# Kernel optimization log

Hardware: AMD Instinct MI355X
Metric: run time of the kernel (lower is better)

Reference implementation:

```python
import jax, jax.numpy as jnp
import numpy as np

# ---- configuration matching init_kwargs ----
D_IN, D_HID, D_OUT = 4096, 4096, 4096
INTRINSIC = 1024            # size of trainable vector V
BATCH = 512
Q = float(min(np.log(60000.0) ** 2 / INTRINSIC, 1.0))  # fastJL_vars: q = min(ln(60000)^2/d, 1)

PARAM_SHAPES = {
    'W1': (D_HID, D_IN),   # nn.Linear weight is (out, in)
    'b1': (D_HID,),
    'W2': (D_OUT, D_HID),
    'b2': (D_OUT,),
}

def _next_pow2(n):
    return 1 << int(np.ceil(np.log2(n)))

def fwht(x):
    """Fast Walsh-Hadamard transform over a length-2^k vector.
    Mirrors fast_walsh_hadamard_torched: at step i, split axis i of the
    [2]*k view into halves a,b and concatenate (a+b, a-b)."""
    n = x.shape[0]
    steps = int(round(np.log2(n)))
    for i in range(steps):
        y = x.reshape(2 ** i, 2, -1)
        a, b = y[:, 0], y[:, 1]
        x = jnp.stack([a + b, a - b], axis=1).reshape(n)
    return x

def fastjl(V, D, PP, shape):
    """ret = (1/dd) * (PP * FWHT(D * pad(V, LL)))[:DD], reshaped to param shape."""
    LL = D.shape[0]
    dd = V.shape[0]
    DD = int(np.prod(shape))
    v_pad = jnp.zeros((LL,), V.dtype).at[:dd].set(V)
    h = fwht(D * v_pad)
    return ((PP * h)[:DD] / dd).reshape(shape)

def setup_inputs() -> dict:
    key = jax.random.key(0)
    ks = jax.random.split(key, 4 + 3 * len(PARAM_SHAPES) + len(PARAM_SHAPES))
    inp = {}
    inp['x'] = jax.random.normal(ks[0], (BATCH, D_IN), dtype=jnp.float32)
    inp['V'] = jax.random.normal(ks[1], (INTRINSIC,), dtype=jnp.float32) * 0.01
    i = 2
    for name, shape in PARAM_SHAPES.items():
        # initial (frozen) parameter values
        scale = 1.0 / np.sqrt(shape[-1]) if len(shape) > 1 else 0.0
        inp[name + '_init'] = jax.random.normal(ks[i], shape, dtype=jnp.float32) * scale
        LL = _next_pow2(int(np.prod(shape)))
        # D: Rademacher +-1
        rad = jax.random.bernoulli(ks[i + 1], 0.5, (LL,))
        inp['D_' + name] = jnp.where(rad, 1.0, -1.0).astype(jnp.float32)
        # PP = B * R, B ~ Bernoulli(1-q), R ~ N(0, (1/q)^2)
        B = jax.random.bernoulli(ks[i + 2], 1.0 - Q, (LL,)).astype(jnp.float32)
        R = jax.random.normal(ks[i + 3], (LL,), dtype=jnp.float32) * (1.0 / Q)
        inp['PP_' + name] = B * R
        i += 4
    return inp

def reference(x, V, W1_init, b1_init, W2_init, b2_init,
              D_W1, PP_W1, D_b1, PP_b1, D_W2, PP_W2, D_b2, PP_b2):
    # Reconstruct each wrapped-module parameter: init + FastJL(V)
    W1 = W1_init + fastjl(V, D_W1, PP_W1, PARAM_SHAPES['W1'])
    b1 = b1_init + fastjl(V, D_b1, PP_b1, PARAM_SHAPES['b1'])
    W2 = W2_init + fastjl(V, D_W2, PP_W2, PARAM_SHAPES['W2'])
    b2 = b2_init + fastjl(V, D_b2, PP_b2, PARAM_SHAPES['b2'])
    # wrapped module forward: Linear -> ReLU -> Linear
    h = jax.nn.relu(x @ W1.T + b1)
    return h @ W2.T + b2
```

## Files before the change

### kernel.cpp

```cpp
#include <hip/hip_runtime.h>
#include <hip/hip_bf16.h>
#include <stdint.h>

typedef unsigned short u16;
typedef __attribute__((ext_vector_type(8))) short short8;
typedef __attribute__((ext_vector_type(4))) float f32x4;

__device__ __forceinline__ uint32_t f2bf(float f) {
    union { float f; uint32_t u; } c; c.f = f;
    uint32_t u = c.u;
    u += 0x7fffu + ((u >> 16) & 1u);
    return u >> 16;
}

__device__ __forceinline__ void glds16(const void* g, void* l) {
    __builtin_amdgcn_global_load_lds(
        (const __attribute__((address_space(1))) uint32_t*)g,
        (__attribute__((address_space(3))) uint32_t*)l,
        16, 0, 0);
}

__device__ __forceinline__ uint2 wrow2(float4 wi, float4 pp, float4 gv) {
    uint32_t lo = f2bf(wi.x + pp.x * gv.x) | (f2bf(wi.y + pp.y * gv.y) << 16);
    uint32_t hi = f2bf(wi.z + pp.z * gv.z) | (f2bf(wi.w + pp.w * gv.w) << 16);
    return make_uint2(lo, hi);
}

__global__ void fwht_g_kernel(const float* __restrict__ V,
                              const float* __restrict__ D0, const float* __restrict__ D1,
                              const float* __restrict__ D2, const float* __restrict__ D3,
                              float* __restrict__ g) {
    __shared__ float s[1024];
    int t = threadIdx.x;
    const float* D = (blockIdx.x == 0) ? D0 : (blockIdx.x == 1) ? D1 :
                     (blockIdx.x == 2) ? D2 : D3;
    s[t] = D[t] * V[t];
    __syncthreads();
    #pragma unroll
    for (int st = 512; st >= 1; st >>= 1) {
        float a = s[t];
        float b = s[t ^ st];
        __syncthreads();
        s[t] = (t & st) ? (b - a) : (a + b);
        __syncthreads();
    }
    g[blockIdx.x * 1024 + t] = s[t] * (1.0f / 1024.0f);
}

__global__ void bias_kernel(const float* __restrict__ init, const float* __restrict__ PP,
                            const float* __restrict__ g, float* __restrict__ out, int n) {
    int i = blockIdx.x * blockDim.x + threadIdx.x;
    if (i < n) out[i] = init[i] + PP[i] * g[i & 1023];
}

__global__ void cast_kernel(const float* __restrict__ in, u16* __restrict__ out, int n4) {
    int i = blockIdx.x * blockDim.x + threadIdx.x;
    if (i >= n4) return;
    float4 v = ((const float4*)in)[i];
    uint32_t lo = f2bf(v.x) | (f2bf(v.y) << 16);
    uint32_t hi = f2bf(v.z) | (f2bf(v.w) << 16);
    ((uint2*)out)[i] = make_uint2(lo, hi);
}

__global__ __launch_bounds__(256, 2) void gemm_fused(const u16* __restrict__ A,
                                                     const float* __restrict__ Winit,
                                                     const float* __restrict__ PP,
                                                     const float* __restrict__ gvec,
                                                     float* __restrict__ P,
                                                     int M, int N, int K, int Kslice) {
    constexpr int BM = 256, BN = 64, BK = 64;
    __shared__ u16 As[2][BM * BK];
    __shared__ u16 Bs[2][BN * BK];

    const int t    = threadIdx.x;
    const int wid  = t >> 6;
    const int lane = t & 63;
    const int fr   = lane & 15;
    const int fq   = lane >> 4;
    const int rx   = (fr & 7) << 4;

    const int bn = blockIdx.x, bm = blockIdx.y, sk = blockIdx.z;
    const int k_beg = sk * Kslice;
    const int kmax  = k_beg + Kslice - BK;
    const int npair = (Kslice / BK) / 2;

    const u16* Abase = A + (size_t)(bm * BM) * K;

    const int rB  = t >> 4;
    const int cB  = (t & 15) * 4;
    const int cb8 = (t & 15) * 8;
    const int wxor = (rB & 7) << 4;
    const float* Wb = Winit + (size_t)(bn * BN + rB) * K;
    const float* Pb = PP    + (size_t)(bn * BN + rB) * K;
    const size_t rstride = (size_t)16 * K;

    float4 w00, w01, w02, w03, p00, p01, p02, p03;
    float4 w10, w11, w12, w13, p10, p11, p12, p13;

#define PF_W0(k0) do {                                        \
        const float* wp_ = Wb + (k0) + cB;                    \
        const float* qp_ = Pb + (k0) + cB;                    \
        w00 = *(const float4*)(wp_);                          \
        w01 = *(const float4*)(wp_ + rstride);                \
        w02 = *(const float4*)(wp_ + 2 * rstride);            \
        w03 = *(const float4*)(wp_ + 3 * rstride);            \
        p00 = *(const float4*)(qp_);                          \
        p01 = *(const float4*)(qp_ + rstride);                \
        p02 = *(const float4*)(qp_ + 2 * rstride);            \
        p03 = *(const float4*)(qp_ + 3 * rstride);            \
    } while (0)

#define PF_W1(k0) do {                                        \
        const float* wp_ = Wb + (k0) + cB;                    \
        const float* qp_ = Pb + (k0) + cB;                    \
        w10 = *(const float4*)(wp_);                          \
        w11 = *(const float4*)(wp_ + rstride);                \
        w12 = *(const float4*)(wp_ + 2 * rstride);            \
        w13 = *(const float4*)(wp_ + 3 * rstride);            \
        p10 = *(const float4*)(qp_);                          \
        p11 = *(const float4*)(qp_ + rstride);                \
        p12 = *(const float4*)(qp_ + 2 * rstride);            \
        p13 = *(const float4*)(qp_ + 3 * rstride);            \
    } while (0)

#define WRITE_B0(k0, buf) do {                                                    \
        float4 gv_ = *(const float4*)(gvec + (((k0) + cB) & 1023));               \
        char* Bp_ = (char*)Bs[buf];                                               \
        *(uint2*)(Bp_ + ((((rB +  0) * 128 + cb8)) ^ wxor)) = wrow2(w00, p00, gv_); \
        *(uint2*)(Bp_ + ((((rB + 16) * 128 + cb8)) ^ wxor)) = wrow2(w01, p01, gv_); \
        *(uint2*)(Bp_ + ((((rB + 32) * 128 + cb8)) ^ wxor)) = wrow2(w02, p02, gv_); \
        *(uint2*)(Bp_ + ((((rB + 48) * 128 + cb8)) ^ wxor)) = wrow2(w03, p03, gv_); \
    } while (0)

#define WRITE_B1(k0, buf) do {                                                    \
        float4 gv_ = *(const float4*)(gvec + (((k0) + cB) & 1023));               \
        char* Bp_ = (char*)Bs[buf];                                               \
        *(uint2*)(Bp_ + ((((rB +  0) * 128 + cb8)) ^ wxor)) = wrow2(w10, p10, gv_); \
        *(uint2*)(Bp_ + ((((rB + 16) * 128 + cb8)) ^ wxor)) = wrow2(w11, p11, gv_); \
        *(uint2*)(Bp_ + ((((rB + 32) * 128 + cb8)) ^ wxor)) = wrow2(w12, p12, gv_); \
        *(uint2*)(Bp_ + ((((rB + 48) * 128 + cb8)) ^ wxor)) = wrow2(w13, p13, gv_); \
    } while (0)

#define STAGE_A(k0, buf) do {                                                     \
        _Pragma("unroll")                                                         \
        for (int q_ = 0; q_ < 8; ++q_) {                                          \
            int L_ = q_ * 256 + t;                           \
            int row_ = L_ >> 3;                                                   \
            int cg_ = (L_ & 7) ^ (row_ & 7);              \
            glds16(Abase + (size_t)row_ * K + (k0) + cg_ * 8, As[buf] + L_ * 8);  \
        }                                                                         \
    } while (0)

#define MFMA_STEP(buf) do {                                                       \
        const char* Ap_ = (const char*)As[buf];                                   \
        const char* Bp_ = (const char*)Bs[buf];                                   \
        __builtin_amdgcn_s_setprio(1);                                            \
        _Pragma("unroll")                                                         \
        for (int ks_ = 0; ks_ < 2; ++ks_) {                                       \
            const int co_ = (ks_ * 64 + fq * 16) ^ rx;                            \
            short8 a_[4], b_[4];                                                  \
            _Pragma("unroll")                                                     \
            for (int m_ = 0; m_ < 4; ++m_)                                        \
                a_[m_] = *(const short8*)(Ap_ +                                   \
                          (wid * 64 + m_ * 16 + fr) * 128 + co_);                 \
            _Pragma("unroll")                                                     \
            for (int n_ = 0; n_ < 4; ++n_)                                        \
                b_[n_] = *(const short8*)(Bp_ + (n_ * 16 + fr) * 128 + co_);      \
            _Pragma("unroll")                                                     \
            for (int m_ = 0; m_ < 4; ++m_)                                        \
                _Pragma("unroll")                                                 \
                for (int n_ = 0; n_ < 4; ++n_)                                    \
                    acc[m_][n_] = __builtin_amdgcn_mfma_f32_16x16x32_bf16(        \
                        a_[m_], b_[n_], acc[m_][n_], 0, 0, 0);                    \
        }                                                                         \
        __builtin_amdgcn_s_setprio(0);                                            \
    } while (0)

#define WAIT_BAR() do {                                                           \
        asm volatile("s_waitcnt vmcnt(8) lgkmcnt(0)" ::: "memory");               \
        __builtin_amdgcn_s_barrier();                                             \
        __builtin_amdgcn_sched_barrier(0);                                        \
    } while (0)

    f32x4 acc[4][4];
    #pragma unroll
    for (int m = 0; m < 4; ++m)
        #pragma unroll
        for (int n = 0; n < 4; ++n)
            acc[m][n] = (f32x4){0.f, 0.f, 0.f, 0.f};

    PF_W0(k_beg);
    __builtin_amdgcn_sched_barrier(0);
    STAGE_A(k_beg, 0);
    __builtin_amdgcn_sched_barrier(0);
    PF_W1(k_beg + BK);
    __builtin_amdgcn_sched_barrier(0);
    WRITE_B0(k_beg, 0);
    WAIT_BAR();

    int kk = k_beg;
    #pragma unroll 1
    for (int p = 0; p < npair; ++p, kk += 2 * BK) {
        const int nk = kk + BK;
        int n2 = kk + 2 * BK; if (n2 > kmax) n2 = kmax;
        int n3 = kk + 3 * BK; if (n3 > kmax) n3 = kmax;

        STAGE_A(nk, 1);
        __builtin_amdgcn_sched_barrier(0);
        PF_W0(n2);
        __builtin_amdgcn_sched_barrier(0);
        MFMA_STEP(0);
        WRITE_B1(nk, 1);
        WAIT_BAR();

        STAGE_A(n2, 0);
        __builtin_amdgcn_sched_barrier(0);
        PF_W1(n3);
        __builtin_amdgcn_sched_barrier(0);
        MFMA_STEP(1);
        WRITE_B0(n2, 0);
        WAIT_BAR();
    }

#undef PF_W0
#undef PF_W1
#undef WRITE_B0
#undef WRITE_B1
#undef STAGE_A
#undef MFMA_STEP
#undef WAIT_BAR

    float* Pp = P + (size_t)sk * M * N;
    #pragma unroll
    for (int m = 0; m < 4; ++m) {
        int grow0 = bm * BM + wid * 64 + m * 16 + fq * 4;
        #pragma unroll
        for (int n = 0; n < 4; ++n) {
            int gcol = bn * BN + n * 16 + fr;
            #pragma unroll
            for (int j = 0; j < 4; ++j)
                Pp[(size_t)(grow0 + j) * N + gcol] = acc[m][n][j];
        }
    }
}

template <typename OutT, bool RELU, int S>
__global__ void reduce_kernel(const float* __restrict__ P, const float* __restrict__ bias,
                              OutT* __restrict__ out, int MN, int N) {
    int i = blockIdx.x * blockDim.x + threadIdx.x;
    if (i * 4 >= MN) return;
    int e = i * 4;
    int col = e & (N - 1);
    float4 acc = ((const float4*)(P + e))[0];
    #pragma unroll
    for (int s = 1; s < S; ++s) {
        float4 p = ((const float4*)(P + (size_t)s * MN + e))[0];
        acc.x += p.x; acc.y += p.y; acc.z += p.z; acc.w += p.w;
    }
    float4 bv = *((const float4*)(bias + col));
    acc.x += bv.x; acc.y += bv.y; acc.z += bv.z; acc.w += bv.w;
    if (RELU) {
        acc.x = fmaxf(acc.x, 0.f); acc.y = fmaxf(acc.y, 0.f);
        acc.z = fmaxf(acc.z, 0.f); acc.w = fmaxf(acc.w, 0.f);
    }
    if constexpr (sizeof(OutT) == 2) {
        uint32_t lo = f2bf(acc.x) | (f2bf(acc.y) << 16);
        uint32_t hi = f2bf(acc.z) | (f2bf(acc.w) << 16);
        ((uint2*)out)[i] = make_uint2(lo, hi);
    } else {
        ((float4*)out)[i] = acc;
    }
}

extern "C" void kernel_launch(void* const* d_in, const int* in_sizes, int n_in,
                              void* d_out, int out_size, void* d_ws, size_t ws_size,
                              hipStream_t stream) {
    (void)in_sizes; (void)n_in; (void)out_size; (void)ws_size;

    const float* x       = (const float*)d_in[0];
    const float* V       = (const float*)d_in[1];
    const float* W1_init = (const float*)d_in[2];
    const float* D_W1    = (const float*)d_in[3];
    const float* PP_W1   = (const float*)d_in[4];
    const float* b1_init = (const float*)d_in[5];
    const float* D_b1    = (const float*)d_in[6];
    const float* PP_b1   = (const float*)d_in[7];
    const float* W2_init = (const float*)d_in[8];
    const float* D_W2    = (const float*)d_in[9];
    const float* PP_W2   = (const float*)d_in[10];
    const float* b2_init = (const float*)d_in[11];
    const float* D_b2    = (const float*)d_in[12];
    const float* PP_b2   = (const float*)d_in[13];

    constexpr size_t MB = 1024 * 1024;
    char* ws = (char*)d_ws;
    float* g    = (float*)(ws);
    float* b1w  = (float*)(ws + 16384);
    float* b2w  = (float*)(ws + 32768);
    u16*   xb   = (u16*)(ws + 65536);
    u16*   hb   = (u16*)(ws + 65536 + 4 * MB);
    float* Pbuf = (float*)(ws + 65536 + 8 * MB);

    const int M = 512, N = 4096, K = 4096, S = 4, Kslice = K / S;

    fwht_g_kernel<<<4, 1024, 0, stream>>>(V, D_W1, D_b1, D_W2, D_b2, g);
    bias_kernel<<<4, 1024, 0, stream>>>(b1_init, PP_b1, g + 1024, b1w, 4096);
    bias_kernel<<<4, 1024, 0, stream>>>(b2_init, PP_b2, g + 3072, b2w, 4096);
    cast_kernel<<<2048, 256, 0, stream>>>(x, xb, M * K / 4);

    gemm_fused<<<dim3(N / 64, M / 256, S), 256, 0, stream>>>(xb, W1_init, PP_W1, g, Pbuf, M, N, K, Kslice);
    reduce_kernel<u16, true, S><<<M * N / 4 / 256, 256, 0, stream>>>(Pbuf, b1w, hb, M * N, N);

    gemm_fused<<<dim3(N / 64, M / 256, S), 256, 0, stream>>>(hb, W2_init, PP_W2, g + 2048, Pbuf, M, N, K, Kslice);
    reduce_kernel<float, false, S><<<M * N / 4 / 256, 256, 0, stream>>>(Pbuf, b2w, (float*)d_out, M * N, N);
}
```

Measured before the change: 130.1 us.

## Halve GEMM M-tile, single-buffer LDS, and raise occupancy to four blocks

Reduces the block tile from 256 to 128 rows, splits warps into a 2x2 layout over the 128x64 tile, and replaces the double-buffered LDS ping-pong with a single buffer guarded by two barriers per K step. Launch bounds are raised to four blocks per CU and the grid doubles in M. The intent is more resident blocks to hide latency, at the cost of each fp32 weight/PP tile being loaded and converted by twice as many blocks and losing the overlap of staging with MFMA.

```diff
diff --git a/kernel.cpp b/kernel.cpp
--- a/kernel.cpp
+++ b/kernel.cpp
@@ -62,27 +62,28 @@
     ((uint2*)out)[i] = make_uint2(lo, hi);
 }
 
-__global__ __launch_bounds__(256, 2) void gemm_fused(const u16* __restrict__ A,
+__global__ __launch_bounds__(256, 4) void gemm_fused(const u16* __restrict__ A,
                                                      const float* __restrict__ Winit,
                                                      const float* __restrict__ PP,
                                                      const float* __restrict__ gvec,
                                                      float* __restrict__ P,
                                                      int M, int N, int K, int Kslice) {
-    constexpr int BM = 256, BN = 64, BK = 64;
-    __shared__ u16 As[2][BM * BK];
-    __shared__ u16 Bs[2][BN * BK];
+    constexpr int BM = 128, BN = 64, BK = 64;
+    __shared__ u16 As[BM * BK];
+    __shared__ u16 Bs[BN * BK];
 
     const int t    = threadIdx.x;
     const int wid  = t >> 6;
     const int lane = t & 63;
+    const int wr   = wid >> 1;
+    const int wc   = wid & 1;
     const int fr   = lane & 15;
     const int fq   = lane >> 4;
     const int rx   = (fr & 7) << 4;
 
     const int bn = blockIdx.x, bm = blockIdx.y, sk = blockIdx.z;
     const int k_beg = sk * Kslice;
-    const int kmax  = k_beg + Kslice - BK;
-    const int npair = (Kslice / BK) / 2;
+    const int nstep = Kslice / BK;
 
     const u16* Abase = A + (size_t)(bm * BM) * K;
 
@@ -94,149 +95,108 @@
     const float* Pb = PP    + (size_t)(bn * BN + rB) * K;
     const size_t rstride = (size_t)16 * K;
 
-    float4 w00, w01, w02, w03, p00, p01, p02, p03;
-    float4 w10, w11, w12, w13, p10, p11, p12, p13;
-
-#define PF_W0(k0) do {                                        \
+    float4 wi0, wi1, wi2, wi3, pp0, pp1, pp2, pp3;
+
+#define PF_W(k0) do {                                         \
         const float* wp_ = Wb + (k0) + cB;                    \
         const float* qp_ = Pb + (k0) + cB;                    \
-        w00 = *(const float4*)(wp_);                          \
-        w01 = *(const float4*)(wp_ + rstride);                \
-        w02 = *(const float4*)(wp_ + 2 * rstride);            \
-        w03 = *(const float4*)(wp_ + 3 * rstride);            \
-        p00 = *(const float4*)(qp_);                          \
-        p01 = *(const float4*)(qp_ + rstride);                \
-        p02 = *(const float4*)(qp_ + 2 * rstride);            \
-        p03 = *(const float4*)(qp_ + 3 * rstride);            \
-    } while (0)
-
-#define PF_W1(k0) do {                                        \
-        const float* wp_ = Wb + (k0) + cB;                    \
-        const float* qp_ = Pb + (k0) + cB;                    \
-        w10 = *(const float4*)(wp_);                          \
-        w11 = *(const float4*)(wp_ + rstride);                \
-        w12 = *(const float4*)(wp_ + 2 * rstride);            \
-        w13 = *(const float4*)(wp_ + 3 * rstride);            \
-        p10 = *(const float4*)(qp_);                          \
-        p11 = *(const float4*)(qp_ + rstride);                \
-        p12 = *(const float4*)(qp_ + 2 * rstride);            \
-        p13 = *(const float4*)(qp_ + 3 * rstride);            \
-    } while (0)
-
-#define WRITE_B0(k0, buf) do {                                                    \
+        wi0 = *(const float4*)(wp_);                          \
+        wi1 = *(const float4*)(wp_ + rstride);                \
+        wi2 = *(const float4*)(wp_ + 2 * rstride);            \
+        wi3 = *(const float4*)(wp_ + 3 * rstride);            \
+        pp0 = *(const float4*)(qp_);                          \
+        pp1 = *(const float4*)(qp_ + rstride);                \
+        pp2 = *(const float4*)(qp_ + 2 * rstride);            \
+        pp3 = *(const float4*)(qp_ + 3 * rstride);            \
+    } while (0)
+
+#define WRITE_B(k0) do {                                                          \
         float4 gv_ = *(const float4*)(gvec + (((k0) + cB) & 1023));               \
-        char* Bp_ = (char*)Bs[buf];                                               \
-        *(uint2*)(Bp_ + ((((rB +  0) * 128 + cb8)) ^ wxor)) = wrow2(w00, p00, gv_); \
-        *(uint2*)(Bp_ + ((((rB + 16) * 128 + cb8)) ^ wxor)) = wrow2(w01, p01, gv_); \
-        *(uint2*)(Bp_ + ((((rB + 32) * 128 + cb8)) ^ wxor)) = wrow2(w02, p02, gv_); \
-        *(uint2*)(Bp_ + ((((rB + 48) * 128 + cb8)) ^ wxor)) = wrow2(w03, p03, gv_); \
-    } while (0)
-
-#define WRITE_B1(k0, buf) do {                                                    \
-        float4 gv_ = *(const float4*)(gvec + (((k0) + cB) & 1023));               \
-        char* Bp_ = (char*)Bs[buf];                                               \
-        *(uint2*)(Bp_ + ((((rB +  0) * 128 + cb8)) ^ wxor)) = wrow2(w10, p10, gv_); \
-        *(uint2*)(Bp_ + ((((rB + 16) * 128 + cb8)) ^ wxor)) = wrow2(w11, p11, gv_); \
-        *(uint2*)(Bp_ + ((((rB + 32) * 128 + cb8)) ^ wxor)) = wrow2(w12, p12, gv_); \
-        *(uint2*)(Bp_ + ((((rB + 48) * 128 + cb8)) ^ wxor)) = wrow2(w13, p13, gv_); \
-    } while (0)
-
-#define STAGE_A(k0, buf) do {                                                     \
+        char* Bp_ = (char*)Bs;                                                    \
+        *(uint2*)(Bp_ + ((((rB +  0) * 128 + cb8)) ^ wxor)) = wrow2(wi0, pp0, gv_); \
+        *(uint2*)(Bp_ + ((((rB + 16) * 128 + cb8)) ^ wxor)) = wrow2(wi1, pp1, gv_); \
+        *(uint2*)(Bp_ + ((((rB + 32) * 128 + cb8)) ^ wxor)) = wrow2(wi2, pp2, gv_); \
+        *(uint2*)(Bp_ + ((((rB + 48) * 128 + cb8)) ^ wxor)) = wrow2(wi3, pp3, gv_); \
+    } while (0)
+
+#define STAGE_A(k0) do {                                                          \
         _Pragma("unroll")                                                         \
-        for (int q_ = 0; q_ < 8; ++q_) {                                          \
+        for (int q_ = 0; q_ < 4; ++q_) {                                          \
             int L_ = q_ * 256 + t;                           \
             int row_ = L_ >> 3;                                                   \
             int cg_ = (L_ & 7) ^ (row_ & 7);              \
-            glds16(Abase + (size_t)row_ * K + (k0) + cg_ * 8, As[buf] + L_ * 8);  \
+            glds16(Abase + (size_t)row_ * K + (k0) + cg_ * 8, As + L_ * 8);       \
         }                                                                         \
     } while (0)
 
-#define MFMA_STEP(buf) do {                                                       \
-        const char* Ap_ = (const char*)As[buf];                                   \
-        const char* Bp_ = (const char*)Bs[buf];                                   \
+#define MFMA_STEP() do {                                                          \
+        const char* Ap_ = (const char*)As;                                        \
+        const char* Bp_ = (const char*)Bs;                                        \
         __builtin_amdgcn_s_setprio(1);                                            \
         _Pragma("unroll")                                                         \
         for (int ks_ = 0; ks_ < 2; ++ks_) {                                       \
             const int co_ = (ks_ * 64 + fq * 16) ^ rx;                            \
-            short8 a_[4], b_[4];                                                  \
+            short8 a_[4], b_[2];                                                  \
             _Pragma("unroll")                                                     \
             for (int m_ = 0; m_ < 4; ++m_)                                        \
                 a_[m_] = *(const short8*)(Ap_ +                                   \
-                          (wid * 64 + m_ * 16 + fr) * 128 + co_);                 \
+                          (wr * 64 + m_ * 16 + fr) * 128 + co_);                  \
             _Pragma("unroll")                                                     \
-            for (int n_ = 0; n_ < 4; ++n_)                                        \
-                b_[n_] = *(const short8*)(Bp_ + (n_ * 16 + fr) * 128 + co_);      \
+            for (int n_ = 0; n_ < 2; ++n_)                                        \
+                b_[n_] = *(const short8*)(Bp_ +                                   \
+                          (wc * 32 + n_ * 16 + fr) * 128 + co_);                  \
             _Pragma("unroll")                                                     \
             for (int m_ = 0; m_ < 4; ++m_)                                        \
                 _Pragma("unroll")                                                 \
-                for (int n_ = 0; n_ < 4; ++n_)                                    \
+                for (int n_ = 0; n_ < 2; ++n_)                                    \
                     acc[m_][n_] = __builtin_amdgcn_mfma_f32_16x16x32_bf16(        \
                         a_[m_], b_[n_], acc[m_][n_], 0, 0, 0);                    \
         }                                                                         \
         __builtin_amdgcn_s_setprio(0);                                            \
     } while (0)
 
-#define WAIT_BAR() do {                                                           \
-        asm volatile("s_waitcnt vmcnt(8) lgkmcnt(0)" ::: "memory");               \
-        __builtin_amdgcn_s_barrier();                                             \
-        __builtin_amdgcn_sched_barrier(0);                                        \
-    } while (0)
-
-    f32x4 acc[4][4];
+    f32x4 acc[4][2];
     #pragma unroll
     for (int m = 0; m < 4; ++m)
         #pragma unroll
-        for (int n = 0; n < 4; ++n)
+        for (int n = 0; n < 2; ++n)
             acc[m][n] = (f32x4){0.f, 0.f, 0.f, 0.f};
 
-    PF_W0(k_beg);
+    PF_W(k_beg);
     __builtin_amdgcn_sched_barrier(0);
-    STAGE_A(k_beg, 0);
-    __builtin_amdgcn_sched_barrier(0);
-    PF_W1(k_beg + BK);
-    __builtin_amdgcn_sched_barrier(0);
-    WRITE_B0(k_beg, 0);
-    WAIT_BAR();
-
-    int kk = k_beg;
+
     #pragma unroll 1
-    for (int p = 0; p < npair; ++p, kk += 2 * BK) {
-        const int nk = kk + BK;
-        int n2 = kk + 2 * BK; if (n2 > kmax) n2 = kmax;
-        int n3 = kk + 3 * BK; if (n3 > kmax) n3 = kmax;
-
-        STAGE_A(nk, 1);
-        __builtin_amdgcn_sched_barrier(0);
-        PF_W0(n2);
-        __builtin_amdgcn_sched_barrier(0);
-        MFMA_STEP(0);
-        WRITE_B1(nk, 1);
-        WAIT_BAR();
-
-        STAGE_A(n2, 0);
-        __builtin_amdgcn_sched_barrier(0);
-        PF_W1(n3);
-        __builtin_amdgcn_sched_barrier(0);
-        MFMA_STEP(1);
-        WRITE_B0(n2, 0);
-        WAIT_BAR();
-    }
-
-#undef PF_W0
-#undef PF_W1
-#undef WRITE_B0
-#undef WRITE_B1
+    for (int s = 0; s < nstep; ++s) {
+        const int k0 = k_beg + s * BK;
+        const int kn = (s + 1 < nstep) ? (k0 + BK) : k_beg;
+
+        STAGE_A(k0);
+        __builtin_amdgcn_sched_barrier(0);
+        WRITE_B(k0);
+        __builtin_amdgcn_sched_barrier(0);
+        PF_W(kn);
+        __builtin_amdgcn_sched_barrier(0);
+        asm volatile("s_waitcnt vmcnt(8) lgkmcnt(0)" ::: "memory");
+        __builtin_amdgcn_s_barrier();
+        __builtin_amdgcn_sched_barrier(0);
+        MFMA_STEP();
+        __builtin_amdgcn_sched_barrier(0);
+        __builtin_amdgcn_s_barrier();
+        __builtin_amdgcn_sched_barrier(0);
+    }
+
+#undef PF_W
+#undef WRITE_B
 #undef STAGE_A
 #undef MFMA_STEP
-#undef WAIT_BAR
 
     float* Pp = P + (size_t)sk * M * N;
     #pragma unroll
     for (int m = 0; m < 4; ++m) {
-        int grow0 = bm * BM + wid * 64 + m * 16 + fq * 4;
+        int grow0 = bm * BM + wr * 64 + m * 16 + fq * 4;
         #pragma unroll
-        for (int n = 0; n < 4; ++n) {
-            int gcol = bn * BN + n * 16 + fr;
+        for (int n = 0; n < 2; ++n) {
+            int gcol = bn * BN + wc * 32 + n * 16 + fr;
             #pragma unroll
             for (int j = 0; j < 4; ++j)
                 Pp[(size_t)(grow0 + j) * N + gcol] = acc[m][n][j];
@@ -308,9 +268,9 @@
     bias_kernel<<<4, 1024, 0, stream>>>(b2_init, PP_b2, g + 3072, b2w, 4096);
     cast_kernel<<<2048, 256, 0, stream>>>(x, xb, M * K / 4);
 
-    gemm_fused<<<dim3(N / 64, M / 256, S), 256, 0, stream>>>(xb, W1_init, PP_W1, g, Pbuf, M, N, K, Kslice);
+    gemm_fused<<<dim3(N / 64, M / 128, S), 256, 0, stream>>>(xb, W1_init, PP_W1, g, Pbuf, M, N, K, Kslice);
     reduce_kernel<u16, true, S><<<M * N / 4 / 256, 256, 0, stream>>>(Pbuf, b1w, hb, M * N, N);
 
-    gemm_fused<<<dim3(N / 64, M / 256, S), 256, 0, stream>>>(hb, W2_init, PP_W2, g + 2048, Pbuf, M, N, K, Kslice);
+    gemm_fused<<<dim3(N / 64, M / 128, S), 256, 0, stream>>>(hb, W2_init, PP_W2, g + 2048, Pbuf, M, N, K, Kslice);
     reduce_kernel<float, false, S><<<M * N / 4 / 256, 256, 0, stream>>>(Pbuf, b2w, (float*)d_out, M * N, N);
 }
```

New measurement: 136.1 us. 4.6% more time.
